# Kernel tuning notes

Hardware: AMD Instinct MI355X
Metric: run time of the kernel (lower is better)

The kernel has to match this reference:

```python
import jax, jax.numpy as jnp
import numpy as np

C = 128       # in_channels
B = 256       # number of graph pairs (inter.shape[0])
N1_PER = 32   # nodes per graph, side 1
N2_PER = 32   # nodes per graph, side 2


def prelu(x, s):
    return jnp.where(x >= 0, x, s * x)


def _lin(k, fan_in, fan_out):
    return jax.random.normal(k, (fan_in, fan_out), jnp.float32) / np.sqrt(fan_in)


def setup_inputs() -> dict:
    key = jax.random.key(0)
    ks = jax.random.split(key, 16)
    N1, N2 = B * N1_PER, B * N2_PER
    d1 = np.full(B, N1_PER, np.int64)
    d2 = np.full(B, N2_PER, np.int64)
    batch_1 = np.repeat(np.arange(B), d1)
    batch_2 = np.repeat(np.arange(B), d2)
    # node offsets per graph (exclusive cumsum)
    s1 = np.concatenate([[0], np.cumsum(d1)[:-1]])
    s2 = np.concatenate([[0], np.cumsum(d2)[:-1]])
    # ragged pairwise cross-product indices, same as the torch loop
    ind_1 = np.concatenate([np.repeat(np.arange(d1[g]), d2[g]) + s1[g] for g in range(B)])
    ind_2 = np.concatenate([np.tile(np.arange(d2[g]), d1[g]) + s1[g] * 0 + s2[g] for g in range(B)])
    batch_ans = np.repeat(np.arange(B), d1 * d2)

    inp = {
        "x_1": jax.random.normal(ks[0], (N1, C), jnp.float32),
        "x_2": jax.random.normal(ks[1], (N2, C), jnp.float32),
        "inter": jax.random.normal(ks[2], (B, C), jnp.float32),
        "batch_1": jnp.asarray(batch_1, jnp.int32),
        "batch_2": jnp.asarray(batch_2, jnp.int32),
        "ind_1": jnp.asarray(ind_1, jnp.int32),
        "ind_2": jnp.asarray(ind_2, jnp.int32),
        "batch_ans": jnp.asarray(batch_ans, jnp.int32),
        # glorot-style param 'a'
        "a": jax.random.normal(ks[3], (C,), jnp.float32) * np.sqrt(2.0 / (1 + C)),
        # mlp: PReLU, Linear(2C,2C), PReLU, Linear(2C,C), PReLU, Linear(C,C)
        "Wm1": _lin(ks[4], 2 * C, 2 * C), "bm1": jnp.zeros((2 * C,), jnp.float32),
        "Wm2": _lin(ks[5], 2 * C, C),     "bm2": jnp.zeros((C,), jnp.float32),
        "Wm3": _lin(ks[6], C, C),         "bm3": jnp.zeros((C,), jnp.float32),
        "pm0": jnp.float32(0.25), "pm1": jnp.float32(0.25), "pm2": jnp.float32(0.25),
        # weight_1: Linear(2C,C), PReLU, Linear(C,1), Sigmoid
        "Wg1a": _lin(ks[7], 2 * C, C), "bg1a": jnp.zeros((C,), jnp.float32),
        "Wg1b": _lin(ks[8], C, 1),     "bg1b": jnp.zeros((1,), jnp.float32),
        "pw1": jnp.float32(0.25),
        # weight_2: Linear(2C,C), PReLU, Linear(C,1), Sigmoid
        "Wg2a": _lin(ks[9], 2 * C, C), "bg2a": jnp.zeros((C,), jnp.float32),
        "Wg2b": _lin(ks[10], C, 1),    "bg2b": jnp.zeros((1,), jnp.float32),
        "pw2": jnp.float32(0.25),
    }
    return inp


def reference(x_1, x_2, inter, batch_1, batch_2, ind_1, ind_2, batch_ans,
              a, Wm1, bm1, Wm2, bm2, Wm3, bm3, pm0, pm1, pm2,
              Wg1a, bg1a, Wg1b, bg1b, pw1, Wg2a, bg2a, Wg2b, bg2b, pw2):
    Bn = inter.shape[0]
    # global_add_pool readouts, broadcast back per node (repeat_interleave == gather by batch id)
    r1 = jax.ops.segment_sum(x_1, batch_1, num_segments=Bn)          # [B, C]
    r2 = jax.ops.segment_sum(x_2, batch_2, num_segments=Bn)          # [B, C]
    x1s = jnp.concatenate([x_1, r2[batch_1]], axis=1)                # [N1, 2C]
    x2s = jnp.concatenate([x_2, r1[batch_2]], axis=1)                # [N2, 2C]
    # gating MLPs -> sigmoid scalar per node
    w1 = jax.nn.sigmoid(prelu(x1s @ Wg1a + bg1a, pw1) @ Wg1b + bg1b)  # [N1, 1]
    w2 = jax.nn.sigmoid(prelu(x2s @ Wg2a + bg2a, pw2) @ Wg2b + bg2b)  # [N2, 1]
    x1g = x_1 * w1
    x2g = x_2 * w2
    # ragged pairwise gather
    xi = x1g[ind_1]                                                  # [P, C]
    xj = x2g[ind_2]                                                  # [P, C]
    h = jnp.concatenate([xi, xj], axis=1)                            # [P, 2C]
    h = prelu(h, pm0) @ Wm1 + bm1
    h = prelu(h, pm1) @ Wm2 + bm2
    h = prelu(h, pm2) @ Wm3 + bm3                                    # [P, C]
    ssi = (a * h) * inter[batch_ans]                                 # [P, C]
    logit = jax.ops.segment_sum(jnp.sum(ssi, axis=-1), batch_ans, num_segments=Bn)  # [B]
    return (logit, xi, xj)
```

## Files before the change

kernel.cpp:

```cpp
#include <hip/hip_runtime.h>
#include <hip/hip_bf16.h>
#include <hip/hip_fp16.h>

typedef __attribute__((ext_vector_type(8))) _Float16 half8;
typedef __attribute__((ext_vector_type(2))) _Float16 f16x2;
typedef __attribute__((ext_vector_type(4))) float f32x4;

#define C_ 128

__device__ __forceinline__ unsigned short f2h(float f) {
    return __builtin_bit_cast(unsigned short, (_Float16)f);
}
__device__ __forceinline__ f16x2 pkrtz(float x, float y) {
    return __builtin_bit_cast(f16x2, __builtin_amdgcn_cvt_pkrtz(x, y));
}
__device__ __forceinline__ float prelu_f(float x, float s) {
    return fmaxf(x, 0.f) + s * fminf(x, 0.f);
}
__device__ __forceinline__ half8 prelu_h8(half8 x, half8 sl) {
    half8 z = {0, 0, 0, 0, 0, 0, 0, 0};
    half8 mx = __builtin_elementwise_max(x, z);
    half8 mn = __builtin_elementwise_min(x, z);
    return mx + mn * sl;
}

__global__ __launch_bounds__(256) void prep_weights(
    const float* __restrict__ Wm1, const float* __restrict__ Wm2,
    const float* __restrict__ Wg1a, const float* __restrict__ Wg2a,
    short* __restrict__ ws)
{
    int tid = blockIdx.x * 256 + threadIdx.x;
    if (tid < 65536) {
        int k = tid >> 8, c = tid & 255;
        ws[c * 256 + k] = (short)f2h(Wm1[tid]);
    }
    if (tid < 32768) {
        int k = tid >> 7, c = tid & 127;
        ws[65536  + c * 256 + k] = (short)f2h(Wm2[tid]);
        ws[98304  + c * 256 + k] = (short)f2h(Wg1a[tid]);
        ws[131072 + c * 256 + k] = (short)f2h(Wg2a[tid]);
    }
}

__global__ __launch_bounds__(256, 1) void interactions_fused(
    const float* __restrict__ x1_, const float* __restrict__ x2_,
    const float* __restrict__ inter, const float* __restrict__ aP,
    const short* __restrict__ Wt,
    const float* __restrict__ bm1, const float* __restrict__ bm2,
    const float* __restrict__ Wm3, const float* __restrict__ bm3,
    const float* __restrict__ pm0p, const float* __restrict__ pm1p,
    const float* __restrict__ pm2p,
    const float* __restrict__ bg1a, const float* __restrict__ Wg1b,
    const float* __restrict__ bg1b, const float* __restrict__ pw1p,
    const float* __restrict__ bg2a, const float* __restrict__ Wg2b,
    const float* __restrict__ bg2b, const float* __restrict__ pw2p,
    float* __restrict__ out)
{
    __shared__ __align__(16) unsigned char regA[33792];
    __shared__ __align__(16) float rr[2][C_];
    __shared__ __align__(16) float tv[C_];
    __shared__ __align__(16) float ugs[C_];
    __shared__ float wgt[2][32];
    __shared__ float red[4];
    __shared__ float cbias_s;

    const int t = threadIdx.x;
    const int g = blockIdx.x;
    const int lane = t & 63;
    const int w = t >> 6;
    float* xs1 = (float*)regA;
    float* xs2 = (float*)(regA + 16896);

    {
        const float* s1 = x1_ + (size_t)g * 4096;
        const float* s2 = x2_ + (size_t)g * 4096;
        #pragma unroll
        for (int q = 0; q < 4; ++q) {
            int idx = q * 256 + t;
            int row = idx >> 5, cc = (idx & 31) * 4;
            float4 v1 = *(const float4*)(s1 + idx * 4);
            float4 v2 = *(const float4*)(s2 + idx * 4);
            *(float4*)(xs1 + row * 132 + cc) = v1;
            *(float4*)(xs2 + row * 132 + cc) = v2;
        }
    }
    __syncthreads();

    if (t < 128) {
        float s = 0.f;
        for (int n = 0; n < 32; ++n) s += xs1[n * 132 + t];
        rr[0][t] = s;
        tv[t] = aP[t] * inter[(size_t)g * C_ + t];
    } else {
        int c = t - 128;
        float s = 0.f;
        for (int n = 0; n < 32; ++n) s += xs2[n * 132 + c];
        rr[1][c] = s;
    }
    __syncthreads();

    if (t < 128) {
        const float* wr = Wm3 + t * C_;
        float s0 = 0, s1 = 0, s2 = 0, s3 = 0;
        #pragma unroll
        for (int k = 0; k < 128; k += 4) {
            float4 wv = *(const float4*)(wr + k);
            s0 += wv.x * tv[k];     s1 += wv.y * tv[k + 1];
            s2 += wv.z * tv[k + 2]; s3 += wv.w * tv[k + 3];
        }
        ugs[t] = (s0 + s1) + (s2 + s3);
    } else if (t < 192) {
        float p = bm3[lane] * tv[lane] + bm3[64 + lane] * tv[64 + lane];
        #pragma unroll
        for (int m = 1; m < 64; m <<= 1) p += __shfl_xor(p, m);
        if (lane == 0) cbias_s = p;
    }

    {
        const int sd = w >> 1;
        const int rt = w & 1;
        const float* xs = sd ? xs2 : xs1;
        const float* roth = sd ? rr[0] : rr[1];
        const short* WgT = Wt + (sd ? 131072 : 98304);
        const float* bga = sd ? bg2a : bg1a;
        const float* wgb = sd ? Wg2b : Wg1b;
        const float bgb = sd ? bg2b[0] : bg1b[0];
        const float pw  = sd ? pw2p[0] : pw1p[0];
        const int row = rt * 16 + (lane & 15);
        const int kg = (lane >> 4) * 8;

        half8 afr[8];
        #pragma unroll
        for (int kt = 0; kt < 8; ++kt) {
            const float* p = (kt < 4) ? (xs + row * 132 + kt * 32 + kg)
                                      : (roth + (kt - 4) * 32 + kg);
            float4 lo = *(const float4*)p;
            float4 hi = *(const float4*)(p + 4);
            f16x2 a = pkrtz(lo.x, lo.y);
            f16x2 b = pkrtz(lo.z, lo.w);
            f16x2 c = pkrtz(hi.x, hi.y);
            f16x2 d = pkrtz(hi.z, hi.w);
            half8 fr = {a[0], a[1], b[0], b[1], c[0], c[1], d[0], d[1]};
            afr[kt] = fr;
        }
        float pr[4] = {0, 0, 0, 0};
        #pragma unroll
        for (int ct = 0; ct < 8; ++ct) {
            const int c = ct * 16 + (lane & 15);
            const short* wp = WgT + c * 256 + kg;
            f32x4 acc = {0, 0, 0, 0};
            #pragma unroll
            for (int kt = 0; kt < 8; ++kt)
                acc = __builtin_amdgcn_mfma_f32_16x16x32_f16(
                          afr[kt], *(const half8*)(wp + kt * 32), acc, 0, 0, 0);
            const float bgac = bga[c], wgbc = wgb[c];
            #pragma unroll
            for (int r = 0; r < 4; ++r)
                pr[r] += prelu_f(acc[r] + bgac, pw) * wgbc;
        }
        #pragma unroll
        for (int r = 0; r < 4; ++r) {
            float p = pr[r];
            p += __shfl_xor(p, 1); p += __shfl_xor(p, 2);
            p += __shfl_xor(p, 4); p += __shfl_xor(p, 8);
            if ((lane & 15) == 0)
                wgt[sd][rt * 16 + (lane >> 4) * 4 + r] =
                    1.f / (1.f + __expf(-(p + bgb)));
        }
    }
    __syncthreads();

    float4 sl1[4], sl2[4];
    {
        const int cc = (t & 31) * 4;
        const int tn = t >> 5;
        #pragma unroll
        for (int m = 0; m < 4; ++m) {
            const int nr = m * 8 + tn;
            const float w1v = wgt[0][nr], w2v = wgt[1][nr];
            float4 v1 = *(float4*)(xs1 + nr * 132 + cc);
            float4 v2 = *(float4*)(xs2 + nr * 132 + cc);
            v1.x *= w1v; v1.y *= w1v; v1.z *= w1v; v1.w *= w1v;
            v2.x *= w2v; v2.y *= w2v; v2.z *= w2v; v2.w *= w2v;
            *(float4*)(xs1 + nr * 132 + cc) = v1;
            *(float4*)(xs2 + nr * 132 + cc) = v2;
            sl1[m] = v1; sl2[m] = v2;
        }
    }
    __syncthreads();

    {
        const int sd = w >> 1;
        const int rt = w & 1;
        const float* xs = sd ? xs2 : xs1;
        const float pm0 = pm0p[0];
        const int row = rt * 16 + (lane & 15);
        const int kg = (lane >> 4) * 8;
        half8 afr[4];
        #pragma unroll
        for (int kt = 0; kt < 4; ++kt) {
            const float* p = xs + row * 132 + kt * 32 + kg;
            float4 lo = *(const float4*)p;
            float4 hi = *(const float4*)(p + 4);
            f16x2 a = pkrtz(prelu_f(lo.x, pm0), prelu_f(lo.y, pm0));
            f16x2 b = pkrtz(prelu_f(lo.z, pm0), prelu_f(lo.w, pm0));
            f16x2 c = pkrtz(prelu_f(hi.x, pm0), prelu_f(hi.y, pm0));
            f16x2 d = pkrtz(prelu_f(hi.z, pm0), prelu_f(hi.w, pm0));
            half8 fr = {a[0], a[1], b[0], b[1], c[0], c[1], d[0], d[1]};
            afr[kt] = fr;
        }
        f32x4 acc[16];
        #pragma unroll
        for (int ct = 0; ct < 16; ++ct) {
            const int c = ct * 16 + (lane & 15);
            const short* wp = Wt + c * 256 + sd * 128 + kg;
            f32x4 av = {0, 0, 0, 0};
            #pragma unroll
            for (int kt = 0; kt < 4; ++kt)
                av = __builtin_amdgcn_mfma_f32_16x16x32_f16(
                         afr[kt], *(const half8*)(wp + kt * 32), av, 0, 0, 0);
            acc[ct] = av;
        }
        __syncthreads();
        unsigned char* dst = regA + (sd ? 16896 : 0);
        #pragma unroll
        for (int ct = 0; ct < 16; ++ct) {
            const int c = ct * 16 + (lane & 15);
            const float badd = sd ? 0.f : bm1[c];
            #pragma unroll
            for (int r = 0; r < 4; ++r) {
                const int n = rt * 16 + (lane >> 4) * 4 + r;
                const int off = n * 512 + ((2 * c + ((n & 7) << 6)) & 511);
                *(unsigned short*)(dst + off) = f2h(acc[ct][r] + badd);
            }
        }
    }
    __syncthreads();

    {
        const float pm1v = pm1p[0], pm2v = pm2p[0];
        const _Float16 pm1s = (_Float16)pm1v;
        const half8 pm1h = {pm1s, pm1s, pm1s, pm1s, pm1s, pm1s, pm1s, pm1s};
        const int cl = lane & 15;
        const int kg8 = (lane >> 4) * 8;
        const int kg16 = kg8 * 2;
        const int c0 = (2 * w) * 16 + cl, c1 = (2 * w + 1) * 16 + cl;
        half8 Bf0[8], Bf1[8];
        const short* w2p0 = Wt + 65536 + c0 * 256 + kg8;
        const short* w2p1 = Wt + 65536 + c1 * 256 + kg8;
        #pragma unroll
        for (int kt = 0; kt < 8; ++kt) {
            Bf0[kt] = *(const half8*)(w2p0 + kt * 32);
            Bf1[kt] = *(const half8*)(w2p1 + kt * 32);
        }
        const float bm2c0 = bm2[c0], bm2c1 = bm2[c1];
        const float ug0 = ugs[c0], ug1 = ugs[c1];
        const unsigned char* Ub = regA;
        const unsigned char* Vb = regA + 16896;

        half8 VrA[8], VrB[8];
        {
            const int j0 = cl, j1 = 16 + cl;
            const int vs = (cl & 7) << 6;
            #pragma unroll
            for (int kt = 0; kt < 8; ++kt) {
                const int koff = kt * 64 + kg16;
                VrA[kt] = *(const half8*)(Vb + j0 * 512 + ((koff + vs) & 511));
                VrB[kt] = *(const half8*)(Vb + j1 * 512 + ((koff + ((j1 & 7) << 6)) & 511));
            }
        }

        float* oxi = out + 256 + (size_t)g * 131072;
        float* oxj = out + 256 + 33554432 + (size_t)g * 131072;
        const int cc = (t & 31) * 4;
        const int tn = t >> 5;
        float psum = 0.f;

#define JSET(VR, JJ)                                                          \
        do {                                                                  \
            f32x4 acc0 = {0, 0, 0, 0}, acc1 = {0, 0, 0, 0};                   \
            _Pragma("unroll")                                                 \
            for (int kt = 0; kt < 8; ++kt) {                                  \
                half8 sfull = u8[kt] + VR[kt];                                \
                half8 af = prelu_h8(sfull, pm1h);                             \
                acc0 = __builtin_amdgcn_mfma_f32_16x16x32_f16(af, Bf0[kt], acc0, 0, 0, 0); \
                acc1 = __builtin_amdgcn_mfma_f32_16x16x32_f16(af, Bf1[kt], acc1, 0, 0, 0); \
            }                                                                 \
            _Pragma("unroll")                                                 \
            for (int r = 0; r < 4; ++r) {                                     \
                psum += prelu_f(acc0[r] + bm2c0, pm2v) * ug0;                 \
                psum += prelu_f(acc1[r] + bm2c1, pm2v) * ug1;                 \
            }                                                                 \
            {                                                                 \
                const int jj_ = (JJ);                                         \
                *(float4*)(oxi + (size_t)(n0 * 32 + jj_) * 128 + cc) = s1a;   \
                *(float4*)(oxi + (size_t)(n1 * 32 + jj_) * 128 + cc) = s1b;   \
                *(float4*)(oxj + (size_t)(jj_ * 32 + n0) * 128 + cc) = s2a;   \
                *(float4*)(oxj + (size_t)(jj_ * 32 + n1) * 128 + cc) = s2b;   \
            }                                                                 \
        } while (0)

        #pragma unroll
        for (int rh = 0; rh < 2; ++rh) {
            const int n0 = rh * 16 + tn;
            const int n1 = rh * 16 + 8 + tn;
            const float4 s1a = sl1[rh * 2], s1b = sl1[rh * 2 + 1];
            const float4 s2a = sl2[rh * 2], s2b = sl2[rh * 2 + 1];
            #pragma unroll 2
            for (int ii = 0; ii < 16; ++ii) {
                const int i = rh * 16 + ii;
                const int ub = i * 512, us = (i & 7) << 6;
                half8 u8[8];
                #pragma unroll
                for (int kt = 0; kt < 8; ++kt)
                    u8[kt] = *(const half8*)(Ub + ub + ((kt * 64 + kg16 + us) & 511));
                JSET(VrA, 2 * ii);
                JSET(VrB, 2 * ii + 1);
            }
        }
#undef JSET
        #pragma unroll
        for (int m = 1; m < 64; m <<= 1) psum += __shfl_xor(psum, m);
        if (lane == 0) red[w] = psum;
    }
    __syncthreads();
    if (t == 0)
        out[g] = red[0] + red[1] + red[2] + red[3] + 1024.f * cbias_s;
}

extern "C" void kernel_launch(void* const* d_in, const int* in_sizes, int n_in,
                              void* d_out, int out_size, void* d_ws, size_t ws_size,
                              hipStream_t stream) {
    const float* x1   = (const float*)d_in[0];
    const float* x2   = (const float*)d_in[1];
    const float* itr  = (const float*)d_in[2];
    const float* a    = (const float*)d_in[8];
    const float* Wm1  = (const float*)d_in[9];
    const float* bm1  = (const float*)d_in[10];
    const float* Wm2  = (const float*)d_in[11];
    const float* bm2  = (const float*)d_in[12];
    const float* Wm3  = (const float*)d_in[13];
    const float* bm3  = (const float*)d_in[14];
    const float* pm0  = (const float*)d_in[15];
    const float* pm1  = (const float*)d_in[16];
    const float* pm2  = (const float*)d_in[17];
    const float* Wg1a = (const float*)d_in[18];
    const float* bg1a = (const float*)d_in[19];
    const float* Wg1b = (const float*)d_in[20];
    const float* bg1b = (const float*)d_in[21];
    const float* pw1  = (const float*)d_in[22];
    const float* Wg2a = (const float*)d_in[23];
    const float* bg2a = (const float*)d_in[24];
    const float* Wg2b = (const float*)d_in[25];
    const float* bg2b = (const float*)d_in[26];
    const float* pw2  = (const float*)d_in[27];
    float* out = (float*)d_out;
    short* Wt = (short*)d_ws;

    hipLaunchKernelGGL(prep_weights, dim3(256), dim3(256), 0, stream,
                       Wm1, Wm2, Wg1a, Wg2a, Wt);
    hipLaunchKernelGGL(interactions_fused, dim3(256), dim3(256), 0, stream,
                       x1, x2, itr, a, Wt, bm1, bm2, Wm3, bm3,
                       pm0, pm1, pm2, bg1a, Wg1b, bg1b, pw1,
                       bg2a, Wg2b, bg2b, pw2, out);
}
```

Baseline: 86.99 us.

## Split each graph across two blocks by j-half and reduce partial logits

The fused kernel now launches two blocks per graph, each handling half of the j (side-2) nodes. This doubles the grid to 512 blocks and permits two blocks per CU through the launch bounds. Per-block partial logits go to a workspace buffer and a new small kernel sums each pair. The prologue (staging, gating MLPs, first layer) is now duplicated in both blocks, and the change adds an extra kernel launch. The weight-prep kernel is also rewritten to write short8 vectors contiguously, and it launches far fewer blocks.

```diff
diff --git a/kernel.cpp b/kernel.cpp
--- a/kernel.cpp
+++ b/kernel.cpp
@@ -4,6 +4,7 @@
 
 typedef __attribute__((ext_vector_type(8))) _Float16 half8;
 typedef __attribute__((ext_vector_type(2))) _Float16 f16x2;
+typedef __attribute__((ext_vector_type(8))) short short8;
 typedef __attribute__((ext_vector_type(4))) float f32x4;
 
 #define C_ 128
@@ -21,7 +22,7 @@
     half8 z = {0, 0, 0, 0, 0, 0, 0, 0};
     half8 mx = __builtin_elementwise_max(x, z);
     half8 mn = __builtin_elementwise_min(x, z);
-    return mx + mn * sl;
+    return mn * sl + mx;
 }
 
 __global__ __launch_bounds__(256) void prep_weights(
@@ -29,20 +30,37 @@
     const float* __restrict__ Wg1a, const float* __restrict__ Wg2a,
     short* __restrict__ ws)
 {
-    int tid = blockIdx.x * 256 + threadIdx.x;
-    if (tid < 65536) {
-        int k = tid >> 8, c = tid & 255;
-        ws[c * 256 + k] = (short)f2h(Wm1[tid]);
-    }
-    if (tid < 32768) {
-        int k = tid >> 7, c = tid & 127;
-        ws[65536  + c * 256 + k] = (short)f2h(Wm2[tid]);
-        ws[98304  + c * 256 + k] = (short)f2h(Wg1a[tid]);
-        ws[131072 + c * 256 + k] = (short)f2h(Wg2a[tid]);
-    }
-}
-
-__global__ __launch_bounds__(256, 1) void interactions_fused(
+    int id = blockIdx.x * 256 + threadIdx.x;
+    if (id < 8192) {
+        int c = id >> 5, kb = (id & 31) * 8;
+        short8 v;
+        #pragma unroll
+        for (int e = 0; e < 8; ++e) v[e] = (short)f2h(Wm1[(kb + e) * 256 + c]);
+        *(short8*)(ws + c * 256 + kb) = v;
+    }
+    if (id < 4096) {
+        int c = id >> 5, kb = (id & 31) * 8;
+        short8 a, b, d;
+        #pragma unroll
+        for (int e = 0; e < 8; ++e) {
+            a[e] = (short)f2h(Wm2 [(kb + e) * C_ + c]);
+            b[e] = (short)f2h(Wg1a[(kb + e) * C_ + c]);
+            d[e] = (short)f2h(Wg2a[(kb + e) * C_ + c]);
+        }
+        *(short8*)(ws + 65536  + c * 256 + kb) = a;
+        *(short8*)(ws + 98304  + c * 256 + kb) = b;
+        *(short8*)(ws + 131072 + c * 256 + kb) = d;
+    }
+}
+
+__global__ __launch_bounds__(256) void reduce_out(
+    const float* __restrict__ part, float* __restrict__ out)
+{
+    int t = threadIdx.x;
+    out[t] = part[2 * t] + part[2 * t + 1];
+}
+
+__global__ __launch_bounds__(256, 2) void interactions_fused(
     const float* __restrict__ x1_, const float* __restrict__ x2_,
     const float* __restrict__ inter, const float* __restrict__ aP,
     const short* __restrict__ Wt,
@@ -54,7 +72,7 @@
     const float* __restrict__ bg1b, const float* __restrict__ pw1p,
     const float* __restrict__ bg2a, const float* __restrict__ Wg2b,
     const float* __restrict__ bg2b, const float* __restrict__ pw2p,
-    float* __restrict__ out)
+    float* __restrict__ part, float* __restrict__ out)
 {
     __shared__ __align__(16) unsigned char regA[33792];
     __shared__ __align__(16) float rr[2][C_];
@@ -65,7 +83,8 @@
     __shared__ float cbias_s;
 
     const int t = threadIdx.x;
-    const int g = blockIdx.x;
+    const int g = blockIdx.x >> 1;
+    const int jh = blockIdx.x & 1;
     const int lane = t & 63;
     const int w = t >> 6;
     float* xs1 = (float*)regA;
@@ -258,15 +277,14 @@
         const unsigned char* Ub = regA;
         const unsigned char* Vb = regA + 16896;
 
-        half8 VrA[8], VrB[8];
+        half8 Vr[8];
         {
-            const int j0 = cl, j1 = 16 + cl;
-            const int vs = (cl & 7) << 6;
+            const int j0 = jh * 16 + cl;
+            const int vs = (j0 & 7) << 6;
             #pragma unroll
             for (int kt = 0; kt < 8; ++kt) {
                 const int koff = kt * 64 + kg16;
-                VrA[kt] = *(const half8*)(Vb + j0 * 512 + ((koff + vs) & 511));
-                VrB[kt] = *(const half8*)(Vb + j1 * 512 + ((koff + ((j1 & 7) << 6)) & 511));
+                Vr[kt] = *(const half8*)(Vb + j0 * 512 + ((koff + vs) & 511));
             }
         }
 
@@ -275,30 +293,6 @@
         const int cc = (t & 31) * 4;
         const int tn = t >> 5;
         float psum = 0.f;
-
-#define JSET(VR, JJ)                                                          \
-        do {                                                                  \
-            f32x4 acc0 = {0, 0, 0, 0}, acc1 = {0, 0, 0, 0};                   \
-            _Pragma("unroll")                                                 \
-            for (int kt = 0; kt < 8; ++kt) {                                  \
-                half8 sfull = u8[kt] + VR[kt];                                \
-                half8 af = prelu_h8(sfull, pm1h);                             \
-                acc0 = __builtin_amdgcn_mfma_f32_16x16x32_f16(af, Bf0[kt], acc0, 0, 0, 0); \
-                acc1 = __builtin_amdgcn_mfma_f32_16x16x32_f16(af, Bf1[kt], acc1, 0, 0, 0); \
-            }                                                                 \
-            _Pragma("unroll")                                                 \
-            for (int r = 0; r < 4; ++r) {                                     \
-                psum += prelu_f(acc0[r] + bm2c0, pm2v) * ug0;                 \
-                psum += prelu_f(acc1[r] + bm2c1, pm2v) * ug1;                 \
-            }                                                                 \
-            {                                                                 \
-                const int jj_ = (JJ);                                         \
-                *(float4*)(oxi + (size_t)(n0 * 32 + jj_) * 128 + cc) = s1a;   \
-                *(float4*)(oxi + (size_t)(n1 * 32 + jj_) * 128 + cc) = s1b;   \
-                *(float4*)(oxj + (size_t)(jj_ * 32 + n0) * 128 + cc) = s2a;   \
-                *(float4*)(oxj + (size_t)(jj_ * 32 + n1) * 128 + cc) = s2b;   \
-            }                                                                 \
-        } while (0)
 
         #pragma unroll
         for (int rh = 0; rh < 2; ++rh) {
@@ -314,18 +308,32 @@
                 #pragma unroll
                 for (int kt = 0; kt < 8; ++kt)
                     u8[kt] = *(const half8*)(Ub + ub + ((kt * 64 + kg16 + us) & 511));
-                JSET(VrA, 2 * ii);
-                JSET(VrB, 2 * ii + 1);
+                f32x4 acc0 = {0, 0, 0, 0}, acc1 = {0, 0, 0, 0};
+                #pragma unroll
+                for (int kt = 0; kt < 8; ++kt) {
+                    half8 af = prelu_h8(u8[kt] + Vr[kt], pm1h);
+                    acc0 = __builtin_amdgcn_mfma_f32_16x16x32_f16(af, Bf0[kt], acc0, 0, 0, 0);
+                    acc1 = __builtin_amdgcn_mfma_f32_16x16x32_f16(af, Bf1[kt], acc1, 0, 0, 0);
+                }
+                #pragma unroll
+                for (int r = 0; r < 4; ++r) {
+                    psum += prelu_f(acc0[r] + bm2c0, pm2v) * ug0;
+                    psum += prelu_f(acc1[r] + bm2c1, pm2v) * ug1;
+                }
+                const int jj = jh * 16 + ii;
+                *(float4*)(oxi + (size_t)(n0 * 32 + jj) * 128 + cc) = s1a;
+                *(float4*)(oxi + (size_t)(n1 * 32 + jj) * 128 + cc) = s1b;
+                *(float4*)(oxj + (size_t)(jj * 32 + n0) * 128 + cc) = s2a;
+                *(float4*)(oxj + (size_t)(jj * 32 + n1) * 128 + cc) = s2b;
             }
         }
-#undef JSET
         #pragma unroll
         for (int m = 1; m < 64; m <<= 1) psum += __shfl_xor(psum, m);
         if (lane == 0) red[w] = psum;
     }
     __syncthreads();
     if (t == 0)
-        out[g] = red[0] + red[1] + red[2] + red[3] + 1024.f * cbias_s;
+        part[blockIdx.x] = red[0] + red[1] + red[2] + red[3] + 512.f * cbias_s;
 }
 
 extern "C" void kernel_launch(void* const* d_in, const int* in_sizes, int n_in,
@@ -356,11 +364,14 @@
     const float* pw2  = (const float*)d_in[27];
     float* out = (float*)d_out;
     short* Wt = (short*)d_ws;
-
-    hipLaunchKernelGGL(prep_weights, dim3(256), dim3(256), 0, stream,
+    float* part = (float*)(Wt + 163840);
+
+    hipLaunchKernelGGL(prep_weights, dim3(32), dim3(256), 0, stream,
                        Wm1, Wm2, Wg1a, Wg2a, Wt);
-    hipLaunchKernelGGL(interactions_fused, dim3(256), dim3(256), 0, stream,
+    hipLaunchKernelGGL(interactions_fused, dim3(512), dim3(256), 0, stream,
                        x1, x2, itr, a, Wt, bm1, bm2, Wm3, bm3,
                        pm0, pm1, pm2, bg1a, Wg1b, bg1b, pw1,
-                       bg2a, Wg2b, bg2b, pw2, out);
-}
+                       bg2a, Wg2b, bg2b, pw2, part, out);
+    hipLaunchKernelGGL(reduce_out, dim3(1), dim3(256), 0, stream,
+                       part, out);
+}
```

Result: slower. 92.86 us (+6.7%).
